# Optimization experiments

Measured on AMD Instinct MI355X. Metric: run time of the kernel, lower is better.

Reference implementation:

```python
import jax, jax.numpy as jnp
import numpy as np

N_ENTITIES = 4096
FEATURE_DIM = 512
CELLS = 39
PAIRS = 8192


def setup_inputs() -> dict:
    key = jax.random.key(0)
    k_emb, k_idx, k_wg, k_wl = jax.random.split(key, 4)
    embedding = jax.random.normal(k_emb, (N_ENTITIES, FEATURE_DIM), dtype=jnp.float32)
    index = jax.random.randint(k_idx, (CELLS, PAIRS, 2), 0, N_ENTITIES, dtype=jnp.int32)
    # kaiming_uniform-style scale for the global bilinear weight
    bound_g = np.sqrt(6.0 / FEATURE_DIM)
    weights_global = jax.random.uniform(k_wg, (FEATURE_DIM, FEATURE_DIM), minval=-bound_g, maxval=bound_g, dtype=jnp.float32)
    # per-cell diagonal scaling vectors (original stores them as [d,1] params)
    weights_local = jax.random.uniform(k_wl, (CELLS, FEATURE_DIM), minval=-bound_g, maxval=bound_g, dtype=jnp.float32)
    return {"embedding": embedding, "index": index,
            "weights_global": weights_global, "weights_local": weights_local}


def reference(embedding, index, weights_global, weights_local):
    # Original per-cell math: einsum('bn,nm,mj,jk,bk->b', A, diag(wl), W, diag(wl), B)
    # diag(wl) @ ... is just elementwise scaling of the gathered embeddings, so:
    #   out[c,p] = sum_{n,k} (A[c,p,n]*wl[c,n]) * W[n,k] * (B[c,p,k]*wl[c,k])
    wl = weights_local[:, None, :]                      # [C,1,d]
    A = embedding[index[..., 0]] * wl                   # [C,P,d]
    B = embedding[index[..., 1]] * wl                   # [C,P,d]
    return jnp.einsum('cpn,nk,cpk->cp', A, weights_global, B)  # [C,P]
```

## Files before the change

kernel.cpp:

```cpp
#include <hip/hip_runtime.h>
#include <stdint.h>

#define NE 4096
#define FD 512
#define NCELLS 39
#define NPAIRS 8192
#define NT (FD / 64)

typedef __attribute__((ext_vector_type(8))) short short8;
typedef __attribute__((ext_vector_type(8))) unsigned short ushort8;
typedef __attribute__((ext_vector_type(4))) float f32x4;
typedef __attribute__((ext_vector_type(4))) unsigned int uint4v;

__device__ __forceinline__ unsigned short f2bf(float f) {
  union { float f; uint32_t u; } v; v.f = f;
  uint32_t u = v.u;
  return (unsigned short)((u + 0x7fffu + ((u >> 16) & 1u)) >> 16);
}
__device__ __forceinline__ float bf2f(unsigned short b) {
  return __uint_as_float(((uint32_t)b) << 16);
}

__device__ __forceinline__ void async16(const void* g, void* l) {
  __builtin_amdgcn_global_load_lds((const __attribute__((address_space(1))) void*)g,
                                   (__attribute__((address_space(3))) void*)l, 16, 0, 0);
}

__global__ __launch_bounds__(256) void init_k(const float* __restrict__ E,
                                              unsigned short* __restrict__ Ebf,
                                              const float* __restrict__ W,
                                              const float* __restrict__ wl,
                                              unsigned short* __restrict__ Wt) {
  __shared__ float tile[32][33];
  const int bid = blockIdx.x;
  if (bid < 2048) {
    const int i = bid * 256 + threadIdx.x;
    const float4 v = ((const float4*)E)[i];
    ushort4 o;
    o.x = f2bf(v.x); o.y = f2bf(v.y); o.z = f2bf(v.z); o.w = f2bf(v.w);
    ((ushort4*)Ebf)[i] = o;
    return;
  }
  const int pid = bid - 2048;
  const int ci = pid >> 8;
  const int rem = pid & 255;
  const int tn = (rem & 15) * 32, tk = (rem >> 4) * 32;
  const int tx = threadIdx.x & 31, ty = threadIdx.x >> 5;
  const float* wlr = wl + (size_t)ci * FD;
#pragma unroll
  for (int i = 0; i < 4; i++) {
    int n = tn + ty + i * 8;
    tile[ty + i * 8][tx] = W[(size_t)n * FD + tk + tx] * wlr[n];
  }
  __syncthreads();
  unsigned short* dst = Wt + (size_t)ci * FD * FD;
#pragma unroll
  for (int i = 0; i < 4; i++) {
    int kout = tk + ty + i * 8;
    dst[(size_t)kout * FD + tn + tx] = f2bf(tile[tx][ty + i * 8] * wlr[kout]);
  }
}

__global__ __launch_bounds__(256) void conv_e(const float* __restrict__ E,
                                              unsigned short* __restrict__ Ebf) {
  const int i = blockIdx.x * 256 + threadIdx.x;
  const float4 v = ((const float4*)E)[i];
  ushort4 o;
  o.x = f2bf(v.x); o.y = f2bf(v.y); o.z = f2bf(v.z); o.w = f2bf(v.w);
  ((ushort4*)Ebf)[i] = o;
}

__global__ __launch_bounds__(256) void prep_w(const float* __restrict__ W,
                                              const float* __restrict__ wl,
                                              unsigned short* __restrict__ Wt,
                                              int c0) {
  __shared__ float tile[32][33];
  const int ci = blockIdx.z;
  const int tn = blockIdx.x * 32, tk = blockIdx.y * 32;
  const int tx = threadIdx.x & 31, ty = threadIdx.x >> 5;
  const float* wlr = wl + (size_t)(c0 + ci) * FD;
#pragma unroll
  for (int i = 0; i < 4; i++) {
    int n = tn + ty + i * 8;
    tile[ty + i * 8][tx] = W[(size_t)n * FD + tk + tx] * wlr[n];
  }
  __syncthreads();
  unsigned short* dst = Wt + (size_t)ci * FD * FD;
#pragma unroll
  for (int i = 0; i < 4; i++) {
    int kout = tk + ty + i * 8;
    dst[(size_t)kout * FD + tn + tx] = f2bf(tile[tx][ty + i * 8] * wlr[kout]);
  }
}

__global__ __launch_bounds__(512, 2) void gemm_k(const unsigned short* __restrict__ Ebf,
                                                 const unsigned short* __restrict__ Wt,
                                                 unsigned short* __restrict__ U) {
  __shared__ unsigned short lds[2][2][2][128 * 64];
  const int t = threadIdx.x;
  const int id = blockIdx.x;
  int bx, by, ci;
  if (gridDim.x == 32 * NCELLS) {
    if (id < 1024) {
      const int a = id & 7, m = (id >> 3) & 7, h = (id >> 6) & 3, w = id >> 8;
      bx = m | ((a & 1) << 3);
      const int cb = (w << 4) | ((a >> 1) << 2) | h;
      ci = cb >> 1; by = cb & 1;
    } else {
      const int r = id - 1024;
      bx = r & 15;
      const int cb = 64 + (r >> 4);
      ci = cb >> 1; by = cb & 1;
    }
  } else {
    const int xcd = id & 7;
    const int j = id >> 3;
    bx = xcd * 2 + (j & 1);
    by = (j >> 1) & 1;
    ci = j >> 2;
  }

  const unsigned short* Ag = Ebf + (size_t)bx * 256 * FD;
  const unsigned short* Bg = Wt + (size_t)ci * FD * FD + (size_t)by * 256 * FD;

  const int wave = t >> 6, lane = t & 63;
  const int wm = wave >> 2, wn = wave & 3;
  const int lr = lane & 15, lq = lane >> 4;

  const int pg0 = t, pg1 = 512 + t;
  const int sr0 = pg0 >> 3, sg0 = pg0 & 7;
  const int sr1 = pg1 >> 3, sg1 = pg1 & 7;
  const int soff0 = sr0 * FD + ((sg0 ^ (sr0 & 7)) << 3);
  const int soff1 = sr1 * FD + ((sg1 ^ (sr1 & 7)) << 3);
  const int loff0 = pg0 * 8, loff1 = pg1 * 8;

  const int swz0 = (lq ^ (lr & 7)) << 3;
  const int swz1 = ((4 + lq) ^ (lr & 7)) << 3;

#define STAGE(OP, HALF, KT, GBASE)                                                \
  do {                                                                            \
    const int bi_ = (KT) & 1;                       \
    const int kt_ = (KT) < NT ? (KT) : (NT - 1);       \
    const unsigned short* gb_ = (GBASE) + (size_t)(HALF) * (128 * FD) + kt_ * 64; \
    unsigned short* d_ = &lds[bi_][OP][HALF][0];                                  \
    async16(gb_ + soff0, d_ + loff0);                                             \
    async16(gb_ + soff1, d_ + loff1);                                             \
  } while (0)

  short8 a[8], b01[4], b23[4];
  f32x4 acc[8][4];
#pragma unroll
  for (int i = 0; i < 8; i++)
#pragma unroll
    for (int j2 = 0; j2 < 4; j2++) acc[i][j2] = (f32x4){0.f, 0.f, 0.f, 0.f};

#define LDA(BUF, MSET)                                                  \
  do {                                                                  \
    const unsigned short* p_ = &lds[BUF][0][wm][0];                     \
    _Pragma("unroll") for (int mi_ = 0; mi_ < 4; ++mi_) {               \
      const int row_ = (MSET) * 64 + mi_ * 16 + lr;                     \
      a[mi_ * 2 + 0] = *(const short8*)&p_[row_ * 64 + swz0];           \
      a[mi_ * 2 + 1] = *(const short8*)&p_[row_ * 64 + swz1];           \
    }                                                                   \
  } while (0)

#define LDB(BUF, NSET, DST)                                             \
  do {                                                                  \
    const unsigned short* p_ = &lds[BUF][1][wn >> 1][0];                \
    _Pragma("unroll") for (int ni_ = 0; ni_ < 2; ++ni_) {               \
      const int row_ = (wn & 1) * 64 + ((NSET) * 2 + ni_) * 16 + lr;    \
      (DST)[ni_ * 2 + 0] = *(const short8*)&p_[row_ * 64 + swz0];       \
      (DST)[ni_ * 2 + 1] = *(const short8*)&p_[row_ * 64 + swz1];       \
    }                                                                   \
  } while (0)

#define MMA(MSET, NSET, B)                                                               \
  do {                                                                                   \
    __builtin_amdgcn_s_setprio(1);                                                       \
    _Pragma("unroll") for (int mi_ = 0; mi_ < 4; ++mi_)                                  \
    _Pragma("unroll") for (int ni_ = 0; ni_ < 2; ++ni_)                                  \
    _Pragma("unroll") for (int s_ = 0; s_ < 2; ++s_)                                     \
      acc[(MSET) * 4 + mi_][(NSET) * 2 + ni_] = __builtin_amdgcn_mfma_f32_16x16x32_bf16( \
          a[mi_ * 2 + s_], (B)[ni_ * 2 + s_],                                            \
          acc[(MSET) * 4 + mi_][(NSET) * 2 + ni_], 0, 0, 0);                             \
    __builtin_amdgcn_s_setprio(0);                                                       \
  } while (0)

#define SYNC_LG()                                        \
  do {                                                   \
    __builtin_amdgcn_s_barrier();                        \
    asm volatile("s_waitcnt lgkmcnt(0)" ::: "memory");   \
  } while (0)

  STAGE(1, 0, 0, Bg); STAGE(0, 0, 0, Ag); STAGE(1, 1, 0, Bg); STAGE(0, 1, 0, Ag);
  STAGE(1, 0, 1, Bg); STAGE(0, 0, 1, Ag);
  asm volatile("s_waitcnt vmcnt(4)" ::: "memory");
  __builtin_amdgcn_s_barrier();

  for (int it = 0; it < NT / 2; ++it) {
    const int k1 = 2 * it + 1, k2 = 2 * it + 2, k3 = 2 * it + 3;
    LDA(0, 0); LDB(0, 0, b01);
    STAGE(1, 1, k1, Bg);
    SYNC_LG(); MMA(0, 0, b01); __builtin_amdgcn_s_barrier();
    LDB(0, 1, b23);
    STAGE(0, 1, k1, Ag);
    SYNC_LG(); MMA(0, 1, b23); __builtin_amdgcn_s_barrier();
    LDA(0, 1);
    STAGE(1, 0, k2, Bg);
    SYNC_LG(); MMA(1, 1, b23); __builtin_amdgcn_s_barrier();
    STAGE(0, 0, k2, Ag);
    __builtin_amdgcn_s_barrier();
    MMA(1, 0, b01);
    asm volatile("s_waitcnt vmcnt(4)" ::: "memory");
    __builtin_amdgcn_s_barrier();
    LDA(1, 0); LDB(1, 0, b01);
    STAGE(1, 1, k2, Bg);
    SYNC_LG(); MMA(0, 0, b01); __builtin_amdgcn_s_barrier();
    LDB(1, 1, b23);
    STAGE(0, 1, k2, Ag);
    SYNC_LG(); MMA(0, 1, b23); __builtin_amdgcn_s_barrier();
    LDA(1, 1);
    STAGE(1, 0, k3, Bg);
    SYNC_LG(); MMA(1, 1, b23); __builtin_amdgcn_s_barrier();
    STAGE(0, 0, k3, Ag);
    __builtin_amdgcn_s_barrier();
    MMA(1, 0, b01);
    asm volatile("s_waitcnt vmcnt(4)" ::: "memory");
    __builtin_amdgcn_s_barrier();
  }

  asm volatile("s_waitcnt vmcnt(0)" ::: "memory");
  __syncthreads();
  {
    unsigned short* Ut = &lds[0][0][0][0];
    const int mrow0w = wm * 128, ncol0w = wn * 64;
#pragma unroll
    for (int mi = 0; mi < 8; ++mi)
#pragma unroll
      for (int ni = 0; ni < 4; ++ni)
#pragma unroll
        for (int r = 0; r < 4; ++r) {
          const int row = mrow0w + mi * 16 + lq * 4 + r;
          const int col = ncol0w + ni * 16 + lr;
          Ut[row * 256 + (col ^ ((row & 12) << 2))] = f2bf(acc[mi][ni][r]);
        }
    __syncthreads();
    unsigned short* Up = U + (size_t)ci * NE * FD + (size_t)(bx * 256) * FD + by * 256;
    const int lrow = t >> 5;
    const int le = (t & 31) * 8;
#pragma unroll
    for (int pass = 0; pass < 16; ++pass) {
      const int row = pass * 16 + lrow;
      const ushort8 vv = *(const ushort8*)&Ut[row * 256 + (le ^ ((row & 12) << 2))];
      *(ushort8*)&Up[(size_t)row * FD + le] = vv;
    }
  }
#undef STAGE
#undef LDA
#undef LDB
#undef MMA
#undef SYNC_LG
}

__global__ __launch_bounds__(256) void dot_k(const unsigned short* __restrict__ U,
                                             const unsigned short* __restrict__ Ebf,
                                             const int* __restrict__ index,
                                             float* __restrict__ out,
                                             int c0) {
  const int ci = blockIdx.y;
  const int c = c0 + ci;
  const int wave = threadIdx.x >> 6, lane = threadIdx.x & 63;
  const unsigned short* Uc = U + (size_t)ci * NE * FD;
  const size_t cp = (size_t)c * NPAIRS;
  const int2* idx2 = (const int2*)index + cp;
  float* op = out + cp;
  const int pbase = (blockIdx.x * 4 + wave) * 32;

  const int b1 = lane & 1, b2 = (lane >> 1) & 1, b4 = (lane >> 2) & 1;

  for (int batch = 0; batch < 4; batch++) {
    const int pb = pbase + batch * 8;
    int2 id[8];
#pragma unroll
    for (int b = 0; b < 8; b++) id[b] = idx2[pb + b];
    uint4v uv[8], ev[8];
#pragma unroll
    for (int b = 0; b < 8; b++) {
      uv[b] = *(const uint4v*)(Uc + (size_t)id[b].x * FD + lane * 8);
      ev[b] = *(const uint4v*)(Ebf + (size_t)id[b].y * FD + lane * 8);
    }
    float v[8];
#pragma unroll
    for (int b = 0; b < 8; b++) {
      const ushort8 u = *(const ushort8*)&uv[b];
      const ushort8 e = *(const ushort8*)&ev[b];
      float s = 0.f;
#pragma unroll
      for (int q = 0; q < 8; q++) s += bf2f(u[q]) * bf2f(e[q]);
      v[b] = s;
    }
    float w[4];
#pragma unroll
    for (int q = 0; q < 4; q++) {
      const float keep = b1 ? v[2 * q + 1] : v[2 * q];
      const float send = b1 ? v[2 * q] : v[2 * q + 1];
      w[q] = keep + __shfl_xor(send, 1, 64);
    }
    float u2[2];
#pragma unroll
    for (int q = 0; q < 2; q++) {
      const float keep = b2 ? w[2 * q + 1] : w[2 * q];
      const float send = b2 ? w[2 * q] : w[2 * q + 1];
      u2[q] = keep + __shfl_xor(send, 2, 64);
    }
    float f;
    {
      const float keep = b4 ? u2[1] : u2[0];
      const float send = b4 ? u2[0] : u2[1];
      f = keep + __shfl_xor(send, 4, 64);
    }
    f += __shfl_xor(f, 8, 64);
    f += __shfl_xor(f, 16, 64);
    f += __shfl_xor(f, 32, 64);
    if (lane < 8) op[pb + lane] = f;
  }
}

__global__ __launch_bounds__(256) void naive_k(const float* __restrict__ emb,
                                               const int* __restrict__ index,
                                               const float* __restrict__ W,
                                               const float* __restrict__ wl,
                                               float* __restrict__ out) {
  __shared__ float bs[FD];
  __shared__ float red[256];
  const int c = blockIdx.y, p = blockIdx.x;
  const int i0 = index[((size_t)c * NPAIRS + p) * 2];
  const int i1 = index[((size_t)c * NPAIRS + p) * 2 + 1];
  const float* wlc = wl + (size_t)c * FD;
  for (int k = threadIdx.x; k < FD; k += 256) bs[k] = emb[(size_t)i1 * FD + k] * wlc[k];
  __syncthreads();
  float s = 0.f;
  for (int n = threadIdx.x; n < FD; n += 256) {
    const float* wr = W + (size_t)n * FD;
    float tacc = 0.f;
    for (int k = 0; k < FD; k++) tacc += wr[k] * bs[k];
    s += tacc * emb[(size_t)i0 * FD + n] * wlc[n];
  }
  red[threadIdx.x] = s;
  __syncthreads();
  for (int st = 128; st > 0; st >>= 1) {
    if (threadIdx.x < st) red[threadIdx.x] += red[threadIdx.x + st];
    __syncthreads();
  }
  if (threadIdx.x == 0) out[(size_t)c * NPAIRS + p] = red[0];
}

extern "C" void kernel_launch(void* const* d_in, const int* in_sizes, int n_in,
                              void* d_out, int out_size, void* d_ws, size_t ws_size,
                              hipStream_t stream) {
  const float* emb = (const float*)d_in[0];
  const int* index = (const int*)d_in[1];
  const float* Wg = (const float*)d_in[2];
  const float* wl = (const float*)d_in[3];
  float* out = (float*)d_out;

  const size_t ebytes = (size_t)NE * FD * 2;
  const size_t wtcell = (size_t)FD * FD * 2;
  const size_t ucell = (size_t)NE * FD * 2;
  size_t avail = ws_size > ebytes ? ws_size - ebytes : 0;
  int G = (int)(avail / (wtcell + ucell));
  if (G > NCELLS) G = NCELLS;

  if (G < 1) {
    naive_k<<<dim3(NPAIRS, NCELLS), 256, 0, stream>>>(emb, index, Wg, wl, out);
    return;
  }

  unsigned short* Ebf = (unsigned short*)d_ws;
  unsigned short* Wt = (unsigned short*)((char*)d_ws + ebytes);
  unsigned short* U = (unsigned short*)((char*)d_ws + ebytes + (size_t)G * wtcell);

  if (G >= NCELLS) {
    init_k<<<dim3(2048 + NCELLS * 256), 256, 0, stream>>>(emb, Ebf, Wg, wl, Wt);
    gemm_k<<<dim3(32 * NCELLS), 512, 0, stream>>>(Ebf, Wt, U);
    dot_k<<<dim3(NPAIRS / 128, NCELLS), 256, 0, stream>>>(U, Ebf, index, out, 0);
    return;
  }

  conv_e<<<dim3((NE * FD / 4) / 256), 256, 0, stream>>>(emb, Ebf);
  for (int c0 = 0; c0 < NCELLS; c0 += G) {
    int g = (NCELLS - c0 < G) ? (NCELLS - c0) : G;
    prep_w<<<dim3(FD / 32, FD / 32, g), 256, 0, stream>>>(Wg, wl, Wt, c0);
    gemm_k<<<dim3(32 * g), 512, 0, stream>>>(Ebf, Wt, U);
    dot_k<<<dim3(NPAIRS / 128, g), 256, 0, stream>>>(U, Ebf, index, out, c0);
  }
}
```

Before: 239.9 us.

## Store GEMM output directly and map dot blocks per XCD by cell

The GEMM epilogue no longer stages results through LDS for coalesced 16-byte stores. Each lane now writes bf16 accumulators straight to global memory, which drops two barriers and the LDS round trip but produces scattered 2-byte stores. A new dot kernel replaces the 2D grid with a 1D grid that interleaves block IDs so each XCD handles a fixed set of cells. This aims to keep each cell's U matrix in one XCD's L2 during the gather.

New measurement: 226.8 us. 5.5% less time.

```diff
diff --git a/kernel.cpp b/kernel.cpp
--- a/kernel.cpp
+++ b/kernel.cpp
@@ -229,30 +229,18 @@
     __builtin_amdgcn_s_barrier();
   }
 
-  asm volatile("s_waitcnt vmcnt(0)" ::: "memory");
-  __syncthreads();
-  {
-    unsigned short* Ut = &lds[0][0][0][0];
-    const int mrow0w = wm * 128, ncol0w = wn * 64;
-#pragma unroll
-    for (int mi = 0; mi < 8; ++mi)
-#pragma unroll
-      for (int ni = 0; ni < 4; ++ni)
-#pragma unroll
-        for (int r = 0; r < 4; ++r) {
-          const int row = mrow0w + mi * 16 + lq * 4 + r;
-          const int col = ncol0w + ni * 16 + lr;
-          Ut[row * 256 + (col ^ ((row & 12) << 2))] = f2bf(acc[mi][ni][r]);
-        }
-    __syncthreads();
-    unsigned short* Up = U + (size_t)ci * NE * FD + (size_t)(bx * 256) * FD + by * 256;
-    const int lrow = t >> 5;
-    const int le = (t & 31) * 8;
-#pragma unroll
-    for (int pass = 0; pass < 16; ++pass) {
-      const int row = pass * 16 + lrow;
-      const ushort8 vv = *(const ushort8*)&Ut[row * 256 + (le ^ ((row & 12) << 2))];
-      *(ushort8*)&Up[(size_t)row * FD + le] = vv;
+  unsigned short* Up = U + (size_t)ci * NE * FD;
+  const int mrow0 = bx * 256 + wm * 128;
+  const int ncol0 = by * 256 + wn * 64;
+#pragma unroll
+  for (int mi = 0; mi < 8; ++mi) {
+    const int mbase = mrow0 + mi * 16 + lq * 4;
+#pragma unroll
+    for (int ni = 0; ni < 4; ++ni) {
+      const int n = ncol0 + ni * 16 + lr;
+#pragma unroll
+      for (int r = 0; r < 4; ++r)
+        Up[(size_t)(mbase + r) * FD + n] = f2bf(acc[mi][ni][r]);
     }
   }
 #undef STAGE
@@ -260,6 +248,74 @@
 #undef LDB
 #undef MMA
 #undef SYNC_LG
+}
+
+__global__ __launch_bounds__(256) void dot_p(const unsigned short* __restrict__ U,
+                                             const unsigned short* __restrict__ Ebf,
+                                             const int* __restrict__ index,
+                                             float* __restrict__ out) {
+  const int id = blockIdx.x;
+  const int xcd = id & 7;
+  const int j = id >> 3;
+  const int ci = xcd + 8 * (j >> 6);
+  if (ci >= NCELLS) return;
+  const int pairblock = j & 63;
+
+  const int wave = threadIdx.x >> 6, lane = threadIdx.x & 63;
+  const unsigned short* Uc = U + (size_t)ci * NE * FD;
+  const size_t cp = (size_t)ci * NPAIRS;
+  const int2* idx2 = (const int2*)index + cp;
+  float* op = out + cp;
+  const int pbase = (pairblock * 4 + wave) * 32;
+
+  const int b1 = lane & 1, b2 = (lane >> 1) & 1, b4 = (lane >> 2) & 1;
+
+  for (int batch = 0; batch < 4; batch++) {
+    const int pb = pbase + batch * 8;
+    int2 id8[8];
+#pragma unroll
+    for (int b = 0; b < 8; b++) id8[b] = idx2[pb + b];
+    uint4v uv[8], ev[8];
+#pragma unroll
+    for (int b = 0; b < 8; b++) {
+      uv[b] = *(const uint4v*)(Uc + (size_t)id8[b].x * FD + lane * 8);
+      ev[b] = *(const uint4v*)(Ebf + (size_t)id8[b].y * FD + lane * 8);
+    }
+    float v[8];
+#pragma unroll
+    for (int b = 0; b < 8; b++) {
+      const ushort8 u = *(const ushort8*)&uv[b];
+      const ushort8 e = *(const ushort8*)&ev[b];
+      float s = 0.f;
+#pragma unroll
+      for (int q = 0; q < 8; q++) s += bf2f(u[q]) * bf2f(e[q]);
+      v[b] = s;
+    }
+    float w[4];
+#pragma unroll
+    for (int q = 0; q < 4; q++) {
+      const float keep = b1 ? v[2 * q + 1] : v[2 * q];
+      const float send = b1 ? v[2 * q] : v[2 * q + 1];
+      w[q] = keep + __shfl_xor(send, 1, 64);
+    }
+    float u2[2];
+#pragma unroll
+    for (int q = 0; q < 2; q++) {
+      const float keep = b2 ? w[2 * q + 1] : w[2 * q];
+      const float send = b2 ? w[2 * q] : w[2 * q + 1];
+      u2[q] = keep + __shfl_xor(send, 2, 64);
+    }
+    float f;
+    {
+      const float keep = b4 ? u2[1] : u2[0];
+      const float send = b4 ? u2[0] : u2[1];
+      f = keep + __shfl_xor(send, 4, 64);
+    }
+    f += __shfl_xor(f, 8, 64);
+    f += __shfl_xor(f, 16, 64);
+    f += __shfl_xor(f, 32, 64);
+    if (lane < 8) op[pb + lane] = f;
+  }
 }
 
 __global__ __launch_bounds__(256) void dot_k(const unsigned short* __restrict__ U,
@@ -383,7 +439,7 @@
   if (G >= NCELLS) {
     init_k<<<dim3(2048 + NCELLS * 256), 256, 0, stream>>>(emb, Ebf, Wg, wl, Wt);
     gemm_k<<<dim3(32 * NCELLS), 512, 0, stream>>>(Ebf, Wt, U);
-    dot_k<<<dim3(NPAIRS / 128, NCELLS), 256, 0, stream>>>(U, Ebf, index, out, 0);
+    dot_p<<<dim3(8 * 320), 256, 0, stream>>>(U, Ebf, index, out);
     return;
   }
 
```
